# Kernel optimization log

Hardware: AMD Instinct MI355X
Metric: run time of the kernel (lower is better)

The kernel has to match this reference:

```python
import jax, jax.numpy as jnp
import numpy as np

N_HEADS = 4


def setup_inputs() -> dict:
    key = jax.random.key(0)
    ks = jax.random.split(key, 6)
    B, T, N, D = 4, 16, 64, 256
    x = jax.random.normal(ks[0], (B, T, N, D), dtype=jnp.float32)
    bias_features = jax.random.normal(ks[1], (B, T, N, N, D), dtype=jnp.float32)
    mask = jax.random.randint(ks[2], (B, T, N), 0, 2).astype(bool)
    s = 1.0 / np.sqrt(D).astype(np.float32)
    Wqkv = jax.random.normal(ks[3], (D, 3 * D), dtype=jnp.float32) * s
    bqkv = jnp.zeros((3 * D,), dtype=jnp.float32)
    Wproj = jax.random.normal(ks[4], (D, D), dtype=jnp.float32) * s
    bproj = jnp.zeros((D,), dtype=jnp.float32)
    return {"x": x, "bias_features": bias_features, "mask": mask,
            "Wqkv": Wqkv, "bqkv": bqkv, "Wproj": Wproj, "bproj": bproj}


def reference(x, bias_features, mask, Wqkv, bqkv, Wproj, bproj):
    B, T, N, D = x.shape
    H = N_HEADS
    hd = D // H
    Batch = B * T
    scale = 1.0 / float(np.sqrt(hd))

    x_flat = x.reshape(Batch, N, D)
    qkv = x_flat @ Wqkv + bqkv                      # (Batch, N, 3D)
    q, k, v = jnp.split(qkv, 3, axis=-1)
    q = q.reshape(Batch, N, H, hd).transpose(0, 2, 1, 3)   # (Batch, H, N, hd)
    k = k.reshape(Batch, N, H, hd).transpose(0, 2, 1, 3)
    v = v.reshape(Batch, N, H, hd).transpose(0, 2, 1, 3)

    # geometry bias: (Batch, H, N, N, hd)
    b_geo = bias_features.reshape(Batch, N, N, H, hd).transpose(0, 3, 1, 2, 4)
    # per-pair dot of q[n] with geometry feature for pair (n, m)
    rel_scores = jnp.einsum("bhnd,bhnmd->bhnm", q, b_geo) * scale

    mask_flat = mask.reshape(Batch, 1, 1, N)
    attn_bias = jnp.where(mask_flat, rel_scores, jnp.float32(-1e9))

    scores = jnp.einsum("bhnd,bhmd->bhnm", q, k) * scale + attn_bias
    attn = jax.nn.softmax(scores, axis=-1)
    out = jnp.einsum("bhnm,bhmd->bhnd", attn, v)    # (Batch, H, N, hd)

    out = out.transpose(0, 2, 1, 3).reshape(Batch, N, D)
    out = out @ Wproj + bproj
    return out.reshape(B, T, N, D)
```

## Files before the change

kernel.cpp:

```cpp
#include <hip/hip_runtime.h>
#include <hip/hip_bf16.h>

#define BATCH 64
#define NRES 64
#define DMODEL 256
#define ROWS (BATCH*NRES)
#define QKVC 768
#define SCALE 0.125f
#define LDP 68

typedef float floatx4 __attribute__((ext_vector_type(4)));

__global__ __launch_bounds__(256) void qkv_gemm(
    const float* __restrict__ x, const float* __restrict__ W,
    const float* __restrict__ bq, float* __restrict__ qkv) {
  __shared__ float As[64 * LDP];
  __shared__ float Bs[64 * LDP];
  int t = threadIdx.x;
  int tx = t & 15, ty = t >> 4;
  int rowBase = blockIdx.y * 64;
  int colBase = blockIdx.x * 64;
  float acc[4][4] = {};
  for (int kb = 0; kb < 256; kb += 64) {
#pragma unroll
    for (int p = 0; p < 4; ++p) {
      int e = (p * 256 + t) * 4;
      int r = e >> 6, c = e & 63;
      *(float4*)&As[r * LDP + c] =
          *(const float4*)&x[(size_t)(rowBase + r) * 256 + kb + c];
      *(float4*)&Bs[r * LDP + c] =
          *(const float4*)&W[(size_t)(kb + r) * QKVC + colBase + c];
    }
    __syncthreads();
#pragma unroll 4
    for (int kk = 0; kk < 64; ++kk) {
      float a[4];
      float4 b4 = *(const float4*)&Bs[kk * LDP + tx * 4];
#pragma unroll
      for (int i = 0; i < 4; ++i) a[i] = As[(ty * 4 + i) * LDP + kk];
      float b[4] = {b4.x, b4.y, b4.z, b4.w};
#pragma unroll
      for (int i = 0; i < 4; ++i)
#pragma unroll
        for (int j = 0; j < 4; ++j) acc[i][j] += a[i] * b[j];
    }
    __syncthreads();
  }
#pragma unroll
  for (int i = 0; i < 4; ++i) {
    int r = rowBase + ty * 4 + i;
#pragma unroll
    for (int j = 0; j < 4; ++j) {
      int c = colBase + tx * 4 + j;
      qkv[(size_t)r * QKVC + c] = acc[i][j] + bq[c];
    }
  }
}

__global__ __launch_bounds__(256) void qk_gemm(const float* __restrict__ qkv,
                                               float* __restrict__ qk) {
  __shared__ float qs[64 * 65];
  __shared__ float ks[64 * 65];
  int t = threadIdx.x;
  int bh = blockIdx.x;
  int b = bh >> 2, h = bh & 3;
  for (int i = 0; i < 16; ++i) {
    int idx = i * 256 + t;
    int r = idx >> 6, d = idx & 63;
    qs[r * 65 + d] = qkv[(size_t)(b * 64 + r) * QKVC + h * 64 + d];
    ks[r * 65 + d] = qkv[(size_t)(b * 64 + r) * QKVC + 256 + h * 64 + d];
  }
  __syncthreads();
  int m = t & 63, nq = t >> 6;
  for (int ni = 0; ni < 16; ++ni) {
    int n = nq * 16 + ni;
    float s = 0.f;
#pragma unroll 16
    for (int d = 0; d < 64; ++d) s += qs[n * 65 + d] * ks[m * 65 + d];
    qk[((size_t)bh * 64 + n) * 64 + m] = s;
  }
}

__global__ __launch_bounds__(256) void attn_kernel(
    const float* __restrict__ bias, const int* __restrict__ mask,
    const float* __restrict__ qkv, const float* __restrict__ qk,
    float* __restrict__ ctx) {
  __shared__ float q_s[256];
  __shared__ float rel_s[256];
  __shared__ float attn_s[256];
  int t = threadIdx.x;
  int blk = blockIdx.x;
  int b = blk >> 6;
  int n_res = blk & 63;
  int m = t & 63, h = t >> 6;
  float s_qk = qk[(((size_t)(b * 4 + h) * 64 + n_res) * 64) + m];
  int msk = mask[b * 64 + m];
  q_s[t] = qkv[(size_t)blk * QKVC + t];
  __syncthreads();
  int wave = t >> 6, lane = t & 63;
  int hseg = lane >> 4;
  float4 qv = *(const float4*)&q_s[lane * 4];
  const floatx4* brow_base =
      (const floatx4*)(bias + (size_t)blk * 64 * 256);
#pragma unroll 4
  for (int i = 0; i < 16; ++i) {
    int mm = i * 4 + wave;
    floatx4 bv = __builtin_nontemporal_load(&brow_base[mm * 64 + lane]);
    float p = bv.x * qv.x + bv.y * qv.y + bv.z * qv.z + bv.w * qv.w;
    p += __shfl_xor(p, 1, 64);
    p += __shfl_xor(p, 2, 64);
    p += __shfl_xor(p, 4, 64);
    p += __shfl_xor(p, 8, 64);
    if ((lane & 15) == 0) rel_s[hseg * 64 + mm] = p;
  }
  __syncthreads();
  float rel = rel_s[h * 64 + m];
  float logit = s_qk * SCALE + (msk ? rel * SCALE : -1e9f);
  float mx = logit;
#pragma unroll
  for (int off = 32; off > 0; off >>= 1) mx = fmaxf(mx, __shfl_xor(mx, off, 64));
  float ex = __expf(logit - mx);
  float sm = ex;
#pragma unroll
  for (int off = 32; off > 0; off >>= 1) sm += __shfl_xor(sm, off, 64);
  attn_s[h * 64 + m] = ex / sm;
  __syncthreads();
  int c = t;
  int hh = c >> 6;
  float acc = 0.f;
  const float* vbase = qkv + (size_t)b * 64 * QKVC + 512 + c;
#pragma unroll 8
  for (int mm = 0; mm < 64; ++mm) acc += attn_s[hh * 64 + mm] * vbase[(size_t)mm * QKVC];
  ctx[(size_t)blk * 256 + c] = acc;
}

__global__ __launch_bounds__(256) void proj_gemm(
    const float* __restrict__ ctx, const float* __restrict__ W,
    const float* __restrict__ bp, float* __restrict__ out) {
  __shared__ float As[64 * LDP];
  __shared__ float Bs[64 * LDP];
  int t = threadIdx.x;
  int tx = t & 15, ty = t >> 4;
  int rowBase = blockIdx.y * 64;
  int colBase = blockIdx.x * 64;
  float acc[4][4] = {};
  for (int kb = 0; kb < 256; kb += 64) {
#pragma unroll
    for (int p = 0; p < 4; ++p) {
      int e = (p * 256 + t) * 4;
      int r = e >> 6, c = e & 63;
      *(float4*)&As[r * LDP + c] =
          *(const float4*)&ctx[(size_t)(rowBase + r) * 256 + kb + c];
      *(float4*)&Bs[r * LDP + c] =
          *(const float4*)&W[(size_t)(kb + r) * 256 + colBase + c];
    }
    __syncthreads();
#pragma unroll 4
    for (int kk = 0; kk < 64; ++kk) {
      float a[4];
      float4 b4 = *(const float4*)&Bs[kk * LDP + tx * 4];
#pragma unroll
      for (int i = 0; i < 4; ++i) a[i] = As[(ty * 4 + i) * LDP + kk];
      float b[4] = {b4.x, b4.y, b4.z, b4.w};
#pragma unroll
      for (int i = 0; i < 4; ++i)
#pragma unroll
        for (int j = 0; j < 4; ++j) acc[i][j] += a[i] * b[j];
    }
    __syncthreads();
  }
#pragma unroll
  for (int i = 0; i < 4; ++i) {
    int r = rowBase + ty * 4 + i;
#pragma unroll
    for (int j = 0; j < 4; ++j) {
      int c = colBase + tx * 4 + j;
      out[(size_t)r * 256 + c] = acc[i][j] + bp[c];
    }
  }
}

extern "C" void kernel_launch(void* const* d_in, const int* in_sizes, int n_in,
                              void* d_out, int out_size, void* d_ws, size_t ws_size,
                              hipStream_t stream) {
  const float* x    = (const float*)d_in[0];
  const float* bias = (const float*)d_in[1];
  const int*   mask = (const int*)d_in[2];
  const float* Wqkv = (const float*)d_in[3];
  const float* bqkv = (const float*)d_in[4];
  const float* Wprj = (const float*)d_in[5];
  const float* bprj = (const float*)d_in[6];
  float* out = (float*)d_out;

  float* qkv_ws = (float*)d_ws;
  float* qk_ws  = qkv_ws + (size_t)ROWS * QKVC;
  float* ctx_ws = qk_ws + (size_t)BATCH * 4 * 64 * 64;

  qkv_gemm<<<dim3(12, 64), 256, 0, stream>>>(x, Wqkv, bqkv, qkv_ws);
  qk_gemm<<<256, 256, 0, stream>>>(qkv_ws, qk_ws);
  attn_kernel<<<ROWS, 256, 0, stream>>>(bias, mask, qkv_ws, qk_ws, ctx_ws);
  proj_gemm<<<dim3(4, 64), 256, 0, stream>>>(ctx_ws, Wprj, bprj, out);
}
```

Baseline: 407.4 us.

## Fuse QK score computation into attention kernel and remap bias dot lanes

Removes the separate qk_gemm kernel and its workspace round-trip. The attention kernel now computes the q·k dot products itself alongside the bias dot products. Each lane handles one key row m and a quarter of the feature dimension, and the reductions use fewer shuffles. Each block re-reads K rows from global memory (64 blocks per batch share them), trading one launch and the qk traffic for redundant K loads and a different bias access pattern in which each lane reads strided float4s.

```diff
diff --git a/kernel.cpp b/kernel.cpp
--- a/kernel.cpp
+++ b/kernel.cpp
@@ -57,65 +57,48 @@
   }
 }
 
-__global__ __launch_bounds__(256) void qk_gemm(const float* __restrict__ qkv,
-                                               float* __restrict__ qk) {
-  __shared__ float qs[64 * 65];
-  __shared__ float ks[64 * 65];
-  int t = threadIdx.x;
-  int bh = blockIdx.x;
-  int b = bh >> 2, h = bh & 3;
-  for (int i = 0; i < 16; ++i) {
-    int idx = i * 256 + t;
-    int r = idx >> 6, d = idx & 63;
-    qs[r * 65 + d] = qkv[(size_t)(b * 64 + r) * QKVC + h * 64 + d];
-    ks[r * 65 + d] = qkv[(size_t)(b * 64 + r) * QKVC + 256 + h * 64 + d];
-  }
-  __syncthreads();
-  int m = t & 63, nq = t >> 6;
-  for (int ni = 0; ni < 16; ++ni) {
-    int n = nq * 16 + ni;
-    float s = 0.f;
-#pragma unroll 16
-    for (int d = 0; d < 64; ++d) s += qs[n * 65 + d] * ks[m * 65 + d];
-    qk[((size_t)bh * 64 + n) * 64 + m] = s;
-  }
-}
-
 __global__ __launch_bounds__(256) void attn_kernel(
     const float* __restrict__ bias, const int* __restrict__ mask,
-    const float* __restrict__ qkv, const float* __restrict__ qk,
-    float* __restrict__ ctx) {
+    const float* __restrict__ qkv, float* __restrict__ ctx) {
   __shared__ float q_s[256];
-  __shared__ float rel_s[256];
+  __shared__ float logit_s[256];
   __shared__ float attn_s[256];
   int t = threadIdx.x;
   int blk = blockIdx.x;
   int b = blk >> 6;
-  int n_res = blk & 63;
-  int m = t & 63, h = t >> 6;
-  float s_qk = qk[(((size_t)(b * 4 + h) * 64 + n_res) * 64) + m];
-  int msk = mask[b * 64 + m];
   q_s[t] = qkv[(size_t)blk * QKVC + t];
   __syncthreads();
   int wave = t >> 6, lane = t & 63;
-  int hseg = lane >> 4;
-  float4 qv = *(const float4*)&q_s[lane * 4];
-  const floatx4* brow_base =
-      (const floatx4*)(bias + (size_t)blk * 64 * 256);
-#pragma unroll 4
+  int mi = lane >> 2, di = lane & 3;
+  int m = wave * 16 + mi;
+  int msk = mask[b * 64 + m];
+  const floatx4* brow = (const floatx4*)(bias + (size_t)blk * 64 * 256) + m * 64 + di;
+  const floatx4* krow = (const floatx4*)(qkv + (size_t)(b * 64 + m) * QKVC + 256) + di;
+  const floatx4* qrow = (const floatx4*)q_s + di;
+  float rel[4] = {0.f, 0.f, 0.f, 0.f};
+  float pk[4]  = {0.f, 0.f, 0.f, 0.f};
+#pragma unroll
   for (int i = 0; i < 16; ++i) {
-    int mm = i * 4 + wave;
-    floatx4 bv = __builtin_nontemporal_load(&brow_base[mm * 64 + lane]);
-    float p = bv.x * qv.x + bv.y * qv.y + bv.z * qv.z + bv.w * qv.w;
-    p += __shfl_xor(p, 1, 64);
-    p += __shfl_xor(p, 2, 64);
-    p += __shfl_xor(p, 4, 64);
-    p += __shfl_xor(p, 8, 64);
-    if ((lane & 15) == 0) rel_s[hseg * 64 + mm] = p;
+    floatx4 bv = __builtin_nontemporal_load(&brow[4 * i]);
+    floatx4 kv = krow[4 * i];
+    floatx4 qv = qrow[4 * i];
+    int h = i >> 2;
+    rel[h] += bv.x * qv.x + bv.y * qv.y + bv.z * qv.z + bv.w * qv.w;
+    pk[h]  += kv.x * qv.x + kv.y * qv.y + kv.z * qv.z + kv.w * qv.w;
   }
+#pragma unroll
+  for (int h = 0; h < 4; ++h) {
+    rel[h] += __shfl_xor(rel[h], 1, 64);
+    rel[h] += __shfl_xor(rel[h], 2, 64);
+    pk[h]  += __shfl_xor(pk[h], 1, 64);
+    pk[h]  += __shfl_xor(pk[h], 2, 64);
+  }
+  float myrel = (di == 0) ? rel[0] : (di == 1) ? rel[1] : (di == 2) ? rel[2] : rel[3];
+  float mypk  = (di == 0) ? pk[0]  : (di == 1) ? pk[1]  : (di == 2) ? pk[2]  : pk[3];
+  logit_s[di * 64 + m] = mypk * SCALE + (msk ? myrel * SCALE : -1e9f);
   __syncthreads();
-  float rel = rel_s[h * 64 + m];
-  float logit = s_qk * SCALE + (msk ? rel * SCALE : -1e9f);
+  int h = wave, mm = lane;
+  float logit = logit_s[h * 64 + mm];
   float mx = logit;
 #pragma unroll
   for (int off = 32; off > 0; off >>= 1) mx = fmaxf(mx, __shfl_xor(mx, off, 64));
@@ -123,14 +106,14 @@
   float sm = ex;
 #pragma unroll
   for (int off = 32; off > 0; off >>= 1) sm += __shfl_xor(sm, off, 64);
-  attn_s[h * 64 + m] = ex / sm;
+  attn_s[h * 64 + mm] = ex / sm;
   __syncthreads();
   int c = t;
   int hh = c >> 6;
   float acc = 0.f;
   const float* vbase = qkv + (size_t)b * 64 * QKVC + 512 + c;
 #pragma unroll 8
-  for (int mm = 0; mm < 64; ++mm) acc += attn_s[hh * 64 + mm] * vbase[(size_t)mm * QKVC];
+  for (int k = 0; k < 64; ++k) acc += attn_s[hh * 64 + k] * vbase[(size_t)k * QKVC];
   ctx[(size_t)blk * 256 + c] = acc;
 }
 
@@ -193,11 +176,9 @@
   float* out = (float*)d_out;
 
   float* qkv_ws = (float*)d_ws;
-  float* qk_ws  = qkv_ws + (size_t)ROWS * QKVC;
-  float* ctx_ws = qk_ws + (size_t)BATCH * 4 * 64 * 64;
+  float* ctx_ws = qkv_ws + (size_t)ROWS * QKVC;
 
   qkv_gemm<<<dim3(12, 64), 256, 0, stream>>>(x, Wqkv, bqkv, qkv_ws);
-  qk_gemm<<<256, 256, 0, stream>>>(qkv_ws, qk_ws);
-  attn_kernel<<<ROWS, 256, 0, stream>>>(bias, mask, qkv_ws, qk_ws, ctx_ws);
+  attn_kernel<<<ROWS, 256, 0, stream>>>(bias, mask, qkv_ws, ctx_ws);
   proj_gemm<<<dim3(4, 64), 256, 0, stream>>>(ctx_ws, Wprj, bprj, out);
 }
```

New measurement: 439.6 us. 7.9% more time.
